# Kernel optimization log

Measured on AMD Instinct MI355X. Metric: run time of the kernel, lower is better.

The kernel has to match this reference:

```python
import jax, jax.numpy as jnp
import numpy as np

B, C, H, W = 4, 64, 64, 64
NUM_HEADS = 4
INTER = 64
OUT_PLANE = 64
TOP_K = 5
BN_EPS = 1e-5


def setup_inputs() -> dict:
    key = jax.random.key(0)
    ks = jax.random.split(key, 24)
    d = {}
    d['x'] = jax.random.normal(ks[0], (B, C, H, W), dtype=jnp.float32)
    oc = INTER * NUM_HEADS
    s_in = 1.0 / np.sqrt(C)
    s_oc = 1.0 / np.sqrt(oc)
    s_op = 1.0 / np.sqrt(OUT_PLANE)
    d['wk'] = jax.random.normal(ks[1], (oc, C), dtype=jnp.float32) * s_in
    d['bk'] = jax.random.normal(ks[2], (oc,), dtype=jnp.float32) * s_in
    d['wq'] = jax.random.normal(ks[3], (oc, C), dtype=jnp.float32) * s_in
    d['bq'] = jax.random.normal(ks[4], (oc,), dtype=jnp.float32) * s_in
    d['wv'] = jax.random.normal(ks[5], (oc, C), dtype=jnp.float32) * s_in
    d['bv'] = jax.random.normal(ks[6], (oc,), dtype=jnp.float32) * s_in
    d['wp'] = jax.random.normal(ks[7], (OUT_PLANE, oc), dtype=jnp.float32) * s_oc
    d['bp'] = jax.random.normal(ks[8], (OUT_PLANE,), dtype=jnp.float32) * s_oc
    d['w1'] = jax.random.normal(ks[9], (OUT_PLANE, OUT_PLANE), dtype=jnp.float32) * s_op
    d['b1'] = jax.random.normal(ks[10], (OUT_PLANE,), dtype=jnp.float32) * s_op
    d['w2'] = jax.random.normal(ks[11], (OUT_PLANE, OUT_PLANE), dtype=jnp.float32) * s_op
    d['b2'] = jax.random.normal(ks[12], (OUT_PLANE,), dtype=jnp.float32) * s_op
    d['g1'] = 1.0 + 0.1 * jax.random.normal(ks[13], (OUT_PLANE,), dtype=jnp.float32)
    d['beta1'] = 0.1 * jax.random.normal(ks[14], (OUT_PLANE,), dtype=jnp.float32)
    d['m1'] = 0.1 * jax.random.normal(ks[15], (OUT_PLANE,), dtype=jnp.float32)
    d['v1'] = 1.0 + 0.1 * jax.random.uniform(ks[16], (OUT_PLANE,), dtype=jnp.float32)
    d['g2'] = 1.0 + 0.1 * jax.random.normal(ks[17], (OUT_PLANE,), dtype=jnp.float32)
    d['beta2'] = 0.1 * jax.random.normal(ks[18], (OUT_PLANE,), dtype=jnp.float32)
    d['m2'] = 0.1 * jax.random.normal(ks[19], (OUT_PLANE,), dtype=jnp.float32)
    d['v2'] = 1.0 + 0.1 * jax.random.uniform(ks[20], (OUT_PLANE,), dtype=jnp.float32)
    return d


def _conv1x1(x, w, b):
    return jnp.einsum('bchw,oc->bohw', x, w) + b[None, :, None, None]


def _l2norm(x, axis):
    n = jnp.sqrt(jnp.sum(x * x, axis=axis, keepdims=True))
    return x / jnp.maximum(n, 1e-12)


def _bn(x, g, be, m, v):
    scale = g / jnp.sqrt(v + BN_EPS)
    return (x - m[None, :, None, None]) * scale[None, :, None, None] + be[None, :, None, None]


def _laplacian(topk_idx, feats):
    # topk_idx: (b, N, K) int32; feats: (b, heads, N, F)
    b, heads, N, Fd = feats.shape
    K = topk_idx.shape[-1]
    src = jnp.repeat(jnp.arange(N), K)  # (N*K,)

    def one(idx, f):  # idx (N,K), f (heads,N,F)
        dst = idx.reshape(-1)  # (N*K,)
        # A = topk edges + self-loops; row degrees (dim=1 sum)
        deg = jnp.zeros((N,), feats.dtype).at[src].add(1.0) + 1.0
        norm = jnp.maximum(deg ** -0.5, 1e-9)
        w = norm[src] * norm[dst]  # (N*K,)
        gathered = f[:, dst, :] * w[None, :, None]  # (heads, N*K, F)
        agg = jax.vmap(lambda g_: jnp.zeros((N, Fd), feats.dtype).at[src].add(g_))(gathered)
        # self-loop contribution (value 1, norm[i]^2)
        return agg + (norm * norm)[None, :, None] * f

    return jax.vmap(one)(topk_idx, feats)


def reference(x, wk, bk, wq, bq, wv, bv, wp, bp, w1, b1, w2, b2,
              g1, beta1, m1, v1, g2, beta2, m2, v2):
    b, c, h, w = x.shape
    N = h * w
    # q/k/v: (b, heads, N, inter)
    k = _conv1x1(x, wk, bk).reshape(b, NUM_HEADS, INTER, N).transpose(0, 1, 3, 2)
    q = _conv1x1(x, wq, bq).reshape(b, NUM_HEADS, INTER, N).transpose(0, 1, 3, 2)
    v = _conv1x1(x, wv, bv).reshape(b, NUM_HEADS, INTER, N).transpose(0, 1, 3, 2)
    k = _l2norm(k, -1)
    q = _l2norm(q, -1)
    # hypergraph: cosine similarity over channels, top-k neighbors per node
    x_flat = x.reshape(b, c, N)
    xn = _l2norm(x_flat, 1)
    sim = jnp.einsum('bcn,bcm->bnm', xn, xn)  # (b, N, N)
    _, idx = jax.lax.top_k(sim, TOP_K)  # (b, N, K)
    k = _laplacian(idx, k)
    v = _laplacian(idx, v)
    # hydra attention: kv summed over nodes, broadcast back over q
    kv = jnp.einsum('bhnf,bhnf->bhf', k, v)[:, :, None, :]  # (b, heads, 1, inter)
    hy = q * kv  # (b, heads, N, inter)
    hy = hy.transpose(0, 1, 3, 2).reshape(b, NUM_HEADS * INTER, h, w)
    out = _conv1x1(hy, wp, bp)
    out = jax.nn.relu(_bn(_conv1x1(out, w1, b1), g1, beta1, m1, v1))
    out = jax.nn.relu(_bn(_conv1x1(out, w2, b2), g2, beta2, m2, v2))
    return out
```

## Files before the change

### kernel.cpp

```cpp
#include <hip/hip_runtime.h>
#include <math.h>

#define NB 4
#define NC 64
#define NN 4096
#define NH 4

typedef __attribute__((ext_vector_type(8))) short bf16x8;
typedef __attribute__((ext_vector_type(4))) float f32x4;

__device__ __forceinline__ unsigned int bf16rne(float v) {
    unsigned int u = __float_as_uint(v);
    return (u + 0x7fffu + ((u >> 16) & 1u)) >> 16;
}

__device__ __forceinline__ void ins5k(unsigned int (&tk)[5], unsigned int key) {
    unsigned int n0 = max(tk[0], key);
    unsigned int n1 = min(tk[0], max(tk[1], key));
    unsigned int n2 = min(tk[1], max(tk[2], key));
    unsigned int n3 = min(tk[2], max(tk[3], key));
    unsigned int n4 = min(tk[3], max(tk[4], key));
    tk[0]=n0; tk[1]=n1; tk[2]=n2; tk[3]=n3; tk[4]=n4;
}

__global__ __launch_bounds__(256) void k_xsplit(const float* __restrict__ x,
                                                unsigned short* __restrict__ hl) {
    int t = blockIdx.x*256 + threadIdx.x;
    int b = t >> 12, n = t & (NN-1);
    const float* xb = x + (size_t)b*NC*NN + n;
    float vals[64];
    float ss = 0.f;
    #pragma unroll
    for (int c = 0; c < NC; ++c) { vals[c] = xb[(size_t)c*NN]; ss += vals[c]*vals[c]; }
    float rn = 1.f / fmaxf(sqrtf(ss), 1e-12f);
    unsigned short* ho = hl + (size_t)t*128;
    #pragma unroll
    for (int g = 0; g < 8; ++g) {
        unsigned int hw[4], lw[4];
        #pragma unroll
        for (int p = 0; p < 4; ++p) {
            float v0 = vals[g*8 + p*2]     * rn;
            float v1 = vals[g*8 + p*2 + 1] * rn;
            unsigned int h0 = bf16rne(v0), h1 = bf16rne(v1);
            float r0 = v0 - __uint_as_float(h0 << 16);
            float r1 = v1 - __uint_as_float(h1 << 16);
            unsigned int l0 = bf16rne(r0), l1 = bf16rne(r1);
            hw[p] = h0 | (h1 << 16);
            lw[p] = l0 | (l1 << 16);
        }
        *(uint4*)(ho + g*8)      = make_uint4(hw[0], hw[1], hw[2], hw[3]);
        *(uint4*)(ho + 64 + g*8) = make_uint4(lw[0], lw[1], lw[2], lw[3]);
    }
}

__global__ __launch_bounds__(256) void k_qkv(
    const float* __restrict__ x,
    const float* __restrict__ wk, const float* __restrict__ bk,
    const float* __restrict__ wq, const float* __restrict__ bq,
    const float* __restrict__ wv, const float* __restrict__ bv,
    float* __restrict__ qo, float* __restrict__ ko, float* __restrict__ vo)
{
    int blk = blockIdx.x;
    int nt  = blk & 63;
    int rem = blk >> 6;
    int ot  = rem % 12;
    int b   = rem / 12;
    int mat = ot >> 2, h = ot & 3;
    const float* w    = (mat==0) ? wk : ((mat==1) ? wq : wv);
    const float* bias = (mat==0) ? bk : ((mat==1) ? bq : bv);
    float* outp       = (mat==0) ? ko : ((mat==1) ? qo : vo);

    __shared__ __align__(16) float As[64*68];
    __shared__ __align__(16) float Bs[64*68];
    __shared__ float redq[16][64];
    __shared__ float rnl[64];
    int t = threadIdx.x;
    int n0 = nt*64;
    {
        int f = t >> 2, q4 = t & 3;
        #pragma unroll
        for (int s = 0; s < 4; ++s) {
            int c0 = q4*16 + s*4;
            float4 w4 = *(const float4*)(w + (size_t)(h*64+f)*64 + c0);
            As[(c0+0)*68+f] = w4.x; As[(c0+1)*68+f] = w4.y;
            As[(c0+2)*68+f] = w4.z; As[(c0+3)*68+f] = w4.w;
        }
    }
    {
        int u = t & 15, cb = t >> 4;
        #pragma unroll
        for (int s = 0; s < 4; ++s) {
            int c = cb + 16*s;
            float4 x4 = *(const float4*)(x + ((size_t)b*NC + c)*NN + n0 + u*4);
            *(float4*)&Bs[c*68 + u*4] = x4;
        }
    }
    __syncthreads();
    int tr = t >> 4, tc = t & 15;
    float acc[4][4];
    #pragma unroll
    for (int i=0;i<4;++i) {
        float bb = bias[h*64 + tr*4 + i];
        #pragma unroll
        for (int j=0;j<4;++j) acc[i][j] = bb;
    }
    #pragma unroll 8
    for (int c = 0; c < 64; ++c) {
        float4 a4 = *(const float4*)&As[c*68 + tr*4];
        float4 b4 = *(const float4*)&Bs[c*68 + tc*4];
        float av[4]  = {a4.x,a4.y,a4.z,a4.w};
        float bvv[4] = {b4.x,b4.y,b4.z,b4.w};
        #pragma unroll
        for (int i=0;i<4;++i)
            #pragma unroll
            for (int j=0;j<4;++j)
                acc[i][j] += av[i]*bvv[j];
    }
    if (mat != 2) {
        #pragma unroll
        for (int j=0;j<4;++j) {
            float s2 = acc[0][j]*acc[0][j] + acc[1][j]*acc[1][j]
                     + acc[2][j]*acc[2][j] + acc[3][j]*acc[3][j];
            redq[tr][tc*4+j] = s2;
        }
        __syncthreads();
        if (t < 64) {
            float s2 = 0.f;
            #pragma unroll
            for (int q = 0; q < 16; ++q) s2 += redq[q][t];
            rnl[t] = 1.f / fmaxf(sqrtf(s2), 1e-12f);
        }
        __syncthreads();
        #pragma unroll
        for (int j=0;j<4;++j) {
            float rr = rnl[tc*4+j];
            #pragma unroll
            for (int i=0;i<4;++i) acc[i][j] *= rr;
        }
    }
    float* ob = outp + (((size_t)(b*NH + h))*NN + n0)*64;
    #pragma unroll
    for (int j=0;j<4;++j) {
        float4 o4 = make_float4(acc[0][j], acc[1][j], acc[2][j], acc[3][j]);
        *(float4*)(ob + (size_t)(tc*4+j)*64 + tr*4) = o4;
    }
}

__device__ __forceinline__ void ctile(const bf16x8& ah0, const bf16x8& ah1,
                                      const bf16x8& al0, const bf16x8& al1,
                                      const bf16x8& bh0, const bf16x8& bh1,
                                      const bf16x8& bl0, const bf16x8& bl1,
                                      unsigned int (&tk)[4][5], unsigned int inv)
{
    f32x4 accP = {2.0f, 2.0f, 2.0f, 2.0f};
    f32x4 accQ = {0.f, 0.f, 0.f, 0.f};
    f32x4 accR = {0.f, 0.f, 0.f, 0.f};
    accP = __builtin_amdgcn_mfma_f32_16x16x32_bf16(ah0, bh0, accP, 0,0,0);
    accQ = __builtin_amdgcn_mfma_f32_16x16x32_bf16(al0, bh0, accQ, 0,0,0);
    accR = __builtin_amdgcn_mfma_f32_16x16x32_bf16(ah0, bl0, accR, 0,0,0);
    accP = __builtin_amdgcn_mfma_f32_16x16x32_bf16(ah1, bh1, accP, 0,0,0);
    accQ = __builtin_amdgcn_mfma_f32_16x16x32_bf16(al1, bh1, accQ, 0,0,0);
    accR = __builtin_amdgcn_mfma_f32_16x16x32_bf16(ah1, bl1, accR, 0,0,0);
    #pragma unroll
    for (int r = 0; r < 4; ++r) {
        float v = (accP[r] + accQ[r]) + accR[r];
        unsigned int key = (__float_as_uint(v) & 0xFFFFF000u) | inv;
        ins5k(tk[r], key);
    }
}

__global__ __launch_bounds__(256, 2)
void k_topk(const unsigned short* __restrict__ hl, unsigned int* __restrict__ pk)
{
    int blk = blockIdx.x;
    int cs = blk & 7;
    int rg = (blk >> 3) & 31;
    int b  = blk >> 8;
    int t = threadIdx.x, lane = t & 63, wave = t >> 6;
    int ln = lane & 15, kh = lane >> 4;
    const unsigned short* hb = hl + (size_t)b*NN*128;

    const unsigned short* ap0 = hb + (size_t)(rg*128 + wave*32 + ln)*128 + kh*8;
    const unsigned short* ap1 = ap0 + 16*128;
    bf16x8 a0h0 = *(const bf16x8*)(ap0);
    bf16x8 a0h1 = *(const bf16x8*)(ap0 + 32);
    bf16x8 a0l0 = *(const bf16x8*)(ap0 + 64);
    bf16x8 a0l1 = *(const bf16x8*)(ap0 + 96);
    bf16x8 a1h0 = *(const bf16x8*)(ap1);
    bf16x8 a1h1 = *(const bf16x8*)(ap1 + 32);
    bf16x8 a1l0 = *(const bf16x8*)(ap1 + 64);
    bf16x8 a1l1 = *(const bf16x8*)(ap1 + 96);

    unsigned int tkA[4][5], tkB[4][5];
    #pragma unroll
    for (int r=0;r<4;++r)
        #pragma unroll
        for (int kk=0;kk<5;++kk) { tkA[r][kk] = 0u; tkB[r][kk] = 0u; }

    int colbase = cs*512;
    unsigned int inv0 = 4095u - (unsigned int)(colbase + ln);

    const unsigned short* bp = hb + (size_t)(colbase + ln)*128 + kh*8;
    bf16x8 Ah0 = *(const bf16x8*)(bp);
    bf16x8 Ah1 = *(const bf16x8*)(bp + 32);
    bf16x8 Al0 = *(const bf16x8*)(bp + 64);
    bf16x8 Al1 = *(const bf16x8*)(bp + 96);
    bf16x8 Bh0, Bh1, Bl0, Bl1;

    for (int t5 = 0; t5 < 32; t5 += 2) {
        {
            const unsigned short* p = bp + (size_t)(t5+1)*16*128;
            Bh0 = *(const bf16x8*)(p);
            Bh1 = *(const bf16x8*)(p + 32);
            Bl0 = *(const bf16x8*)(p + 64);
            Bl1 = *(const bf16x8*)(p + 96);
        }
        {
            unsigned int inv = inv0 - (unsigned int)(t5*16);
            ctile(a0h0,a0h1,a0l0,a0l1, Ah0,Ah1,Al0,Al1, tkA, inv);
            ctile(a1h0,a1h1,a1l0,a1l1, Ah0,Ah1,Al0,Al1, tkB, inv);
        }
        {
            int m = (t5+2 < 32) ? (t5+2) : 0;
            const unsigned short* p = bp + (size_t)m*16*128;
            Ah0 = *(const bf16x8*)(p);
            Ah1 = *(const bf16x8*)(p + 32);
            Al0 = *(const bf16x8*)(p + 64);
            Al1 = *(const bf16x8*)(p + 96);
        }
        {
            unsigned int inv = inv0 - (unsigned int)((t5+1)*16);
            ctile(a0h0,a0h1,a0l0,a0l1, Bh0,Bh1,Bl0,Bl1, tkA, inv);
            ctile(a1h0,a1h1,a1l0,a1l1, Bh0,Bh1,Bl0,Bl1, tkB, inv);
        }
    }

    #pragma unroll
    for (int m = 1; m < 16; m <<= 1) {
        #pragma unroll
        for (int r=0;r<4;++r) {
            unsigned int okA[5], okB[5];
            #pragma unroll
            for (int kk=0;kk<5;++kk) {
                okA[kk] = (unsigned int)__shfl_xor((int)tkA[r][kk], m);
                okB[kk] = (unsigned int)__shfl_xor((int)tkB[r][kk], m);
            }
            #pragma unroll
            for (int kk=0;kk<5;++kk) { ins5k(tkA[r], okA[kk]); ins5k(tkB[r], okB[kk]); }
        }
    }
    if (ln == 0) {
        #pragma unroll
        for (int r=0;r<4;++r) {
            int row0 = rg*128 + wave*32 + kh*4 + r;
            size_t base0 = (((size_t)b*NN + row0)*8 + cs)*5;
            size_t base1 = (((size_t)b*NN + row0 + 16)*8 + cs)*5;
            #pragma unroll
            for (int kk=0;kk<5;++kk) { pk[base0+kk] = tkA[r][kk]; pk[base1+kk] = tkB[r][kk]; }
        }
    }
}

__global__ __launch_bounds__(256) void k_kv(const float* __restrict__ ko, const float* __restrict__ vo,
                                            const unsigned int* __restrict__ pk, float* __restrict__ part)
{
    int blk = blockIdx.x;
    int chunk = blk & 15, bh = blk >> 4, b = bh >> 2;
    int t = threadIdx.x;
    __shared__ int idxl[256][5];
    __shared__ float red[4][64];
    {
        int n = chunk*256 + t;
        const uint4* pp = (const uint4*)(pk + ((size_t)b*NN + n)*40);
        unsigned int bk5[5] = {0u,0u,0u,0u,0u};
        #pragma unroll
        for (int e = 0; e < 10; ++e) {
            uint4 v4 = pp[e];
            ins5k(bk5, v4.x); ins5k(bk5, v4.y); ins5k(bk5, v4.z); ins5k(bk5, v4.w);
        }
        #pragma unroll
        for (int kk=0;kk<5;++kk) idxl[t][kk] = 4095 - (int)(bk5[kk] & 0xFFFu);
    }
    __syncthreads();
    int f = t & 63, g = t >> 6;
    const float* kb = ko + (size_t)bh*NN*64;
    const float* vb = vo + (size_t)bh*NN*64;
    float acc = 0.f;
    for (int i2 = 0; i2 < 64; ++i2) {
        int nl = g*64 + i2;
        int n = chunk*256 + nl;
        const int* ip = idxl[nl];
        int j0 = ip[0], j1 = ip[1], j2 = ip[2], j3 = ip[3], j4 = ip[4];
        float lk = kb[(size_t)n*64+f] + kb[(size_t)j0*64+f] + kb[(size_t)j1*64+f]
                 + kb[(size_t)j2*64+f] + kb[(size_t)j3*64+f] + kb[(size_t)j4*64+f];
        float lv = vb[(size_t)n*64+f] + vb[(size_t)j0*64+f] + vb[(size_t)j1*64+f]
                 + vb[(size_t)j2*64+f] + vb[(size_t)j3*64+f] + vb[(size_t)j4*64+f];
        acc += lk*lv;
    }
    red[g][f] = acc;
    __syncthreads();
    if (t < 64) {
        float s2 = red[0][t] + red[1][t] + red[2][t] + red[3][t];
        part[((size_t)bh*64 + t)*16 + chunk] = s2;
    }
}

__global__ __launch_bounds__(256) void k_out(
    const float* __restrict__ qo, const float* __restrict__ wp, const float* __restrict__ part,
    const float* __restrict__ bp,
    const float* __restrict__ w1, const float* __restrict__ b1,
    const float* __restrict__ w2, const float* __restrict__ b2,
    const float* __restrict__ g1, const float* __restrict__ be1,
    const float* __restrict__ m1, const float* __restrict__ v1,
    const float* __restrict__ g2, const float* __restrict__ be2,
    const float* __restrict__ m2, const float* __restrict__ v2,
    float* __restrict__ outp)
{
    int b  = blockIdx.x >> 6;
    int n0 = (blockIdx.x & 63)*64;
    __shared__ __align__(16) float qs[256*68];
    __shared__ __align__(16) float ws2[256*68];
    __shared__ __align__(16) float t0[64*68];
    int t = threadIdx.x;
    {
        int f = t & 63, sub = t >> 6;
        #pragma unroll
        for (int h = 0; h < 4; ++h) {
            const float* qb = qo + (((size_t)(b*4+h))*NN + n0)*64 + f;
            for (int nl = sub; nl < 64; nl += 4)
                qs[(h*64+f)*68 + nl] = qb[(size_t)nl*64];
        }
    }
    {
        const float* pp = part + ((size_t)b*256 + t)*16;
        float s = 0.f;
        #pragma unroll
        for (int c2 = 0; c2 < 16; ++c2) s += pp[c2];
        float kvv = s * (1.f/36.f);
        for (int o = 0; o < 64; ++o)
            ws2[t*68 + o] = wp[(size_t)o*256 + t] * kvv;
    }
    __syncthreads();
    int tr = t >> 4, tc = t & 15;
    float acc[4][4];
    #pragma unroll
    for (int i=0;i<4;++i) {
        float bb = bp[tr*4+i];
        #pragma unroll
        for (int j=0;j<4;++j) acc[i][j] = bb;
    }
    #pragma unroll 8
    for (int hf = 0; hf < 256; ++hf) {
        float4 a4 = *(const float4*)&ws2[hf*68 + tr*4];
        float4 b4 = *(const float4*)&qs[hf*68 + tc*4];
        float av[4]={a4.x,a4.y,a4.z,a4.w}, bvv[4]={b4.x,b4.y,b4.z,b4.w};
        #pragma unroll
        for (int i=0;i<4;++i)
            #pragma unroll
            for (int j=0;j<4;++j)
                acc[i][j] += av[i]*bvv[j];
    }
    #pragma unroll
    for (int i=0;i<4;++i)
        *(float4*)&t0[(tr*4+i)*68 + tc*4] = make_float4(acc[i][0],acc[i][1],acc[i][2],acc[i][3]);
    __syncthreads();
    #pragma unroll
    for (int s = 0; s < 16; ++s) {
        int e = t + 256*s;
        ws2[(e & 63)*68 + (e >> 6)] = w1[e];
    }
    __syncthreads();
    float acc2[4][4];
    #pragma unroll
    for (int i=0;i<4;++i)
        #pragma unroll
        for (int j=0;j<4;++j) acc2[i][j] = 0.f;
    #pragma unroll 8
    for (int c = 0; c < 64; ++c) {
        float4 a4 = *(const float4*)&ws2[c*68 + tr*4];
        float4 b4 = *(const float4*)&t0[c*68 + tc*4];
        float av[4]={a4.x,a4.y,a4.z,a4.w}, bvv[4]={b4.x,b4.y,b4.z,b4.w};
        #pragma unroll
        for (int i=0;i<4;++i)
            #pragma unroll
            for (int j=0;j<4;++j)
                acc2[i][j] += av[i]*bvv[j];
    }
    #pragma unroll
    for (int i=0;i<4;++i) {
        int o = tr*4+i;
        float sc = g1[o] / sqrtf(v1[o] + 1e-5f);
        float bb = b1[o], mm = m1[o], bt = be1[o];
        float4 r;
        r.x = fmaxf((acc2[i][0]+bb-mm)*sc + bt, 0.f);
        r.y = fmaxf((acc2[i][1]+bb-mm)*sc + bt, 0.f);
        r.z = fmaxf((acc2[i][2]+bb-mm)*sc + bt, 0.f);
        r.w = fmaxf((acc2[i][3]+bb-mm)*sc + bt, 0.f);
        *(float4*)&qs[o*68 + tc*4] = r;
    }
    __syncthreads();
    #pragma unroll
    for (int s = 0; s < 16; ++s) {
        int e = t + 256*s;
        ws2[(e & 63)*68 + (e >> 6)] = w2[e];
    }
    __syncthreads();
    float acc3[4][4];
    #pragma unroll
    for (int i=0;i<4;++i)
        #pragma unroll
        for (int j=0;j<4;++j) acc3[i][j] = 0.f;
    #pragma unroll 8
    for (int c = 0; c < 64; ++c) {
        float4 a4 = *(const float4*)&ws2[c*68 + tr*4];
        float4 b4 = *(const float4*)&qs[c*68 + tc*4];
        float av[4]={a4.x,a4.y,a4.z,a4.w}, bvv[4]={b4.x,b4.y,b4.z,b4.w};
        #pragma unroll
        for (int i=0;i<4;++i)
            #pragma unroll
            for (int j=0;j<4;++j)
                acc3[i][j] += av[i]*bvv[j];
    }
    #pragma unroll
    for (int i=0;i<4;++i) {
        int o = tr*4+i;
        float sc = g2[o] / sqrtf(v2[o] + 1e-5f);
        float bb = b2[o], mm = m2[o], bt = be2[o];
        float4 r;
        r.x = fmaxf((acc3[i][0]+bb-mm)*sc + bt, 0.f);
        r.y = fmaxf((acc3[i][1]+bb-mm)*sc + bt, 0.f);
        r.z = fmaxf((acc3[i][2]+bb-mm)*sc + bt, 0.f);
        r.w = fmaxf((acc3[i][3]+bb-mm)*sc + bt, 0.f);
        *(float4*)&t0[o*68 + tc*4] = r;
    }
    __syncthreads();
    float* ob = outp + ((size_t)b*64)*NN + n0;
    #pragma unroll
    for (int s = 0; s < 16; ++s) {
        int e = t + 256*s;
        int o = e >> 6, nl = e & 63;
        ob[(size_t)o*NN + nl] = t0[o*68 + nl];
    }
}

extern "C" void kernel_launch(void* const* d_in, const int* in_sizes, int n_in,
                              void* d_out, int out_size, void* d_ws, size_t ws_size,
                              hipStream_t stream)
{
    (void)in_sizes; (void)n_in; (void)out_size; (void)ws_size;
    const float* x  = (const float*)d_in[0];
    const float* wk = (const float*)d_in[1];
    const float* bk = (const float*)d_in[2];
    const float* wq = (const float*)d_in[3];
    const float* bq = (const float*)d_in[4];
    const float* wv = (const float*)d_in[5];
    const float* bv = (const float*)d_in[6];
    const float* wp = (const float*)d_in[7];
    const float* bp = (const float*)d_in[8];
    const float* w1 = (const float*)d_in[9];
    const float* b1 = (const float*)d_in[10];
    const float* w2 = (const float*)d_in[11];
    const float* b2 = (const float*)d_in[12];
    const float* g1 = (const float*)d_in[13];
    const float* be1= (const float*)d_in[14];
    const float* m1 = (const float*)d_in[15];
    const float* v1 = (const float*)d_in[16];
    const float* g2 = (const float*)d_in[17];
    const float* be2= (const float*)d_in[18];
    const float* m2 = (const float*)d_in[19];
    const float* v2 = (const float*)d_in[20];
    float* out = (float*)d_out;

    float* ws = (float*)d_ws;
    unsigned short* hlb = (unsigned short*)ws;  ws += (size_t)NB*NN*128/2;
    float* qbuf = ws;  ws += (size_t)NB*NH*NN*64;
    float* kbuf = ws;  ws += (size_t)NB*NH*NN*64;
    float* vbuf = ws;  ws += (size_t)NB*NH*NN*64;
    float* part = ws;  ws += (size_t)16*64*16;
    unsigned int* pk = (unsigned int*)ws;  ws += (size_t)NB*NN*40;

    k_xsplit<<<64, 256, 0, stream>>>(x, hlb);
    k_qkv<<<3072, 256, 0, stream>>>(x, wk,bk, wq,bq, wv,bv, qbuf,kbuf,vbuf);
    k_topk<<<1024, 256, 0, stream>>>(hlb, pk);
    k_kv<<<256, 256, 0, stream>>>(kbuf, vbuf, pk, part);
    k_out<<<256, 256, 0, stream>>>(qbuf, wp, part, bp, w1,b1, w2,b2,
                                   g1,be1,m1,v1, g2,be2,m2,v2, out);
}
```

Baseline: 155.2 us.

## Compute QKV projection with split-bf16 MFMA instead of fp32 FMA

```diff
diff --git a/kernel.cpp b/kernel.cpp
--- a/kernel.cpp
+++ b/kernel.cpp
@@ -23,8 +23,51 @@
     tk[0]=n0; tk[1]=n1; tk[2]=n2; tk[3]=n3; tk[4]=n4;
 }
 
+__device__ __forceinline__ void split8(const float* v, uint4& hw4, uint4& lw4) {
+    unsigned int hw[4], lw[4];
+    #pragma unroll
+    for (int p = 0; p < 4; ++p) {
+        float v0 = v[p*2], v1 = v[p*2+1];
+        unsigned int h0 = bf16rne(v0), h1 = bf16rne(v1);
+        float r0 = v0 - __uint_as_float(h0 << 16);
+        float r1 = v1 - __uint_as_float(h1 << 16);
+        unsigned int l0 = bf16rne(r0), l1 = bf16rne(r1);
+        hw[p] = h0 | (h1 << 16);
+        lw[p] = l0 | (l1 << 16);
+    }
+    hw4 = make_uint4(hw[0], hw[1], hw[2], hw[3]);
+    lw4 = make_uint4(lw[0], lw[1], lw[2], lw[3]);
+}
+
 __global__ __launch_bounds__(256) void k_xsplit(const float* __restrict__ x,
-                                                unsigned short* __restrict__ hl) {
+                                                const float* __restrict__ wk,
+                                                const float* __restrict__ wq,
+                                                const float* __restrict__ wv,
+                                                unsigned short* __restrict__ hl,
+                                                unsigned short* __restrict__ xr,
+                                                unsigned short* __restrict__ wsb) {
+    if (blockIdx.x == 64) {
+        int t = threadIdx.x;
+        #pragma unroll
+        for (int rr = 0; rr < 3; ++rr) {
+            int r = t + rr*256;
+            int mat = r >> 8, oc = r & 255;
+            const float* wsrc = (mat==0) ? wk : ((mat==1) ? wq : wv);
+            float wrow[64];
+            #pragma unroll
+            for (int g = 0; g < 16; ++g)
+                *(float4*)&wrow[g*4] = *(const float4*)(wsrc + (size_t)oc*64 + g*4);
+            unsigned short* wo = wsb + (size_t)r*128;
+            #pragma unroll
+            for (int g = 0; g < 8; ++g) {
+                uint4 hw4, lw4;
+                split8(&wrow[g*8], hw4, lw4);
+                *(uint4*)(wo + g*8)      = hw4;
+                *(uint4*)(wo + 64 + g*8) = lw4;
+            }
+        }
+        return;
+    }
     int t = blockIdx.x*256 + threadIdx.x;
     int b = t >> 12, n = t & (NN-1);
     const float* xb = x + (size_t)b*NC*NN + n;
@@ -34,115 +77,92 @@
     for (int c = 0; c < NC; ++c) { vals[c] = xb[(size_t)c*NN]; ss += vals[c]*vals[c]; }
     float rn = 1.f / fmaxf(sqrtf(ss), 1e-12f);
     unsigned short* ho = hl + (size_t)t*128;
+    unsigned short* ro = xr + (size_t)t*128;
     #pragma unroll
     for (int g = 0; g < 8; ++g) {
-        unsigned int hw[4], lw[4];
-        #pragma unroll
-        for (int p = 0; p < 4; ++p) {
-            float v0 = vals[g*8 + p*2]     * rn;
-            float v1 = vals[g*8 + p*2 + 1] * rn;
-            unsigned int h0 = bf16rne(v0), h1 = bf16rne(v1);
-            float r0 = v0 - __uint_as_float(h0 << 16);
-            float r1 = v1 - __uint_as_float(h1 << 16);
-            unsigned int l0 = bf16rne(r0), l1 = bf16rne(r1);
-            hw[p] = h0 | (h1 << 16);
-            lw[p] = l0 | (l1 << 16);
-        }
-        *(uint4*)(ho + g*8)      = make_uint4(hw[0], hw[1], hw[2], hw[3]);
-        *(uint4*)(ho + 64 + g*8) = make_uint4(lw[0], lw[1], lw[2], lw[3]);
-    }
-}
-
-__global__ __launch_bounds__(256) void k_qkv(
-    const float* __restrict__ x,
-    const float* __restrict__ wk, const float* __restrict__ bk,
-    const float* __restrict__ wq, const float* __restrict__ bq,
-    const float* __restrict__ wv, const float* __restrict__ bv,
+        float nv[8];
+        #pragma unroll
+        for (int p = 0; p < 8; ++p) nv[p] = vals[g*8+p] * rn;
+        uint4 hw4, lw4;
+        split8(nv, hw4, lw4);
+        *(uint4*)(ho + g*8)      = hw4;
+        *(uint4*)(ho + 64 + g*8) = lw4;
+        split8(&vals[g*8], hw4, lw4);
+        *(uint4*)(ro + g*8)      = hw4;
+        *(uint4*)(ro + 64 + g*8) = lw4;
+    }
+}
+
+__global__ __launch_bounds__(256, 2) void k_qkv(
+    const unsigned short* __restrict__ xr, const unsigned short* __restrict__ wsb,
+    const float* __restrict__ bk, const float* __restrict__ bq, const float* __restrict__ bv,
     float* __restrict__ qo, float* __restrict__ ko, float* __restrict__ vo)
 {
     int blk = blockIdx.x;
     int nt  = blk & 63;
     int rem = blk >> 6;
-    int ot  = rem % 12;
-    int b   = rem / 12;
-    int mat = ot >> 2, h = ot & 3;
-    const float* w    = (mat==0) ? wk : ((mat==1) ? wq : wv);
+    int mat = rem % 3, b = rem / 3;
     const float* bias = (mat==0) ? bk : ((mat==1) ? bq : bv);
     float* outp       = (mat==0) ? ko : ((mat==1) ? qo : vo);
-
-    __shared__ __align__(16) float As[64*68];
-    __shared__ __align__(16) float Bs[64*68];
-    __shared__ float redq[16][64];
-    __shared__ float rnl[64];
-    int t = threadIdx.x;
-    int n0 = nt*64;
-    {
-        int f = t >> 2, q4 = t & 3;
+    int t = threadIdx.x, lane = t & 63, h = t >> 6;
+    int ln = lane & 15, kh = lane >> 4;
+
+    bf16x8 ah0[4], ah1[4], al0[4], al1[4];
+    const unsigned short* wb2 = wsb + ((size_t)(mat*256 + h*64 + ln))*128 + kh*8;
+    #pragma unroll
+    for (int s = 0; s < 4; ++s) {
+        const unsigned short* p = wb2 + (size_t)s*16*128;
+        ah0[s] = *(const bf16x8*)(p);
+        ah1[s] = *(const bf16x8*)(p + 32);
+        al0[s] = *(const bf16x8*)(p + 64);
+        al1[s] = *(const bf16x8*)(p + 96);
+    }
+    float4 bj[4];
+    #pragma unroll
+    for (int s = 0; s < 4; ++s) bj[s] = *(const float4*)(bias + h*64 + s*16 + kh*4);
+
+    int n0base = nt*64;
+    const unsigned short* xb2 = xr + ((size_t)b*NN + n0base + ln)*128 + kh*8;
+    #pragma unroll
+    for (int j = 0; j < 4; ++j) {
+        const unsigned short* p = xb2 + (size_t)j*16*128;
+        bf16x8 bh0 = *(const bf16x8*)(p);
+        bf16x8 bh1 = *(const bf16x8*)(p + 32);
+        bf16x8 bl0 = *(const bf16x8*)(p + 64);
+        bf16x8 bl1 = *(const bf16x8*)(p + 96);
+        f32x4 av[4];
         #pragma unroll
         for (int s = 0; s < 4; ++s) {
-            int c0 = q4*16 + s*4;
-            float4 w4 = *(const float4*)(w + (size_t)(h*64+f)*64 + c0);
-            As[(c0+0)*68+f] = w4.x; As[(c0+1)*68+f] = w4.y;
-            As[(c0+2)*68+f] = w4.z; As[(c0+3)*68+f] = w4.w;
-        }
-    }
-    {
-        int u = t & 15, cb = t >> 4;
-        #pragma unroll
-        for (int s = 0; s < 4; ++s) {
-            int c = cb + 16*s;
-            float4 x4 = *(const float4*)(x + ((size_t)b*NC + c)*NN + n0 + u*4);
-            *(float4*)&Bs[c*68 + u*4] = x4;
-        }
-    }
-    __syncthreads();
-    int tr = t >> 4, tc = t & 15;
-    float acc[4][4];
-    #pragma unroll
-    for (int i=0;i<4;++i) {
-        float bb = bias[h*64 + tr*4 + i];
-        #pragma unroll
-        for (int j=0;j<4;++j) acc[i][j] = bb;
-    }
-    #pragma unroll 8
-    for (int c = 0; c < 64; ++c) {
-        float4 a4 = *(const float4*)&As[c*68 + tr*4];
-        float4 b4 = *(const float4*)&Bs[c*68 + tc*4];
-        float av[4]  = {a4.x,a4.y,a4.z,a4.w};
-        float bvv[4] = {b4.x,b4.y,b4.z,b4.w};
-        #pragma unroll
-        for (int i=0;i<4;++i)
-            #pragma unroll
-            for (int j=0;j<4;++j)
-                acc[i][j] += av[i]*bvv[j];
-    }
-    if (mat != 2) {
-        #pragma unroll
-        for (int j=0;j<4;++j) {
-            float s2 = acc[0][j]*acc[0][j] + acc[1][j]*acc[1][j]
-                     + acc[2][j]*acc[2][j] + acc[3][j]*acc[3][j];
-            redq[tr][tc*4+j] = s2;
-        }
-        __syncthreads();
-        if (t < 64) {
-            float s2 = 0.f;
-            #pragma unroll
-            for (int q = 0; q < 16; ++q) s2 += redq[q][t];
-            rnl[t] = 1.f / fmaxf(sqrtf(s2), 1e-12f);
-        }
-        __syncthreads();
-        #pragma unroll
-        for (int j=0;j<4;++j) {
-            float rr = rnl[tc*4+j];
-            #pragma unroll
-            for (int i=0;i<4;++i) acc[i][j] *= rr;
-        }
-    }
-    float* ob = outp + (((size_t)(b*NH + h))*NN + n0)*64;
-    #pragma unroll
-    for (int j=0;j<4;++j) {
-        float4 o4 = make_float4(acc[0][j], acc[1][j], acc[2][j], acc[3][j]);
-        *(float4*)(ob + (size_t)(tc*4+j)*64 + tr*4) = o4;
+            f32x4 acc = {bj[s].x, bj[s].y, bj[s].z, bj[s].w};
+            acc = __builtin_amdgcn_mfma_f32_16x16x32_bf16(ah0[s], bh0, acc, 0,0,0);
+            acc = __builtin_amdgcn_mfma_f32_16x16x32_bf16(ah1[s], bh1, acc, 0,0,0);
+            acc = __builtin_amdgcn_mfma_f32_16x16x32_bf16(al0[s], bh0, acc, 0,0,0);
+            acc = __builtin_amdgcn_mfma_f32_16x16x32_bf16(al1[s], bh1, acc, 0,0,0);
+            acc = __builtin_amdgcn_mfma_f32_16x16x32_bf16(ah0[s], bl0, acc, 0,0,0);
+            acc = __builtin_amdgcn_mfma_f32_16x16x32_bf16(ah1[s], bl1, acc, 0,0,0);
+            av[s] = acc;
+        }
+        int n = n0base + j*16 + ln;
+        float* ob = outp + (((size_t)(b*NH + h))*NN + n)*64 + kh*4;
+        if (mat != 2) {
+            float ss = 0.f;
+            #pragma unroll
+            for (int s = 0; s < 4; ++s)
+                ss += av[s][0]*av[s][0] + av[s][1]*av[s][1]
+                    + av[s][2]*av[s][2] + av[s][3]*av[s][3];
+            ss += __shfl_xor(ss, 16);
+            ss += __shfl_xor(ss, 32);
+            float rn = 1.f / fmaxf(sqrtf(ss), 1e-12f);
+            #pragma unroll
+            for (int s = 0; s < 4; ++s)
+                *(float4*)(ob + s*16) = make_float4(av[s][0]*rn, av[s][1]*rn,
+                                                    av[s][2]*rn, av[s][3]*rn);
+        } else {
+            #pragma unroll
+            for (int s = 0; s < 4; ++s)
+                *(float4*)(ob + s*16) = make_float4(av[s][0], av[s][1],
+                                                    av[s][2], av[s][3]);
+        }
     }
 }
 
@@ -473,14 +493,16 @@
 
     float* ws = (float*)d_ws;
     unsigned short* hlb = (unsigned short*)ws;  ws += (size_t)NB*NN*128/2;
+    unsigned short* xrb = (unsigned short*)ws;  ws += (size_t)NB*NN*128/2;
+    unsigned short* wsb = (unsigned short*)ws;  ws += (size_t)768*128/2;
     float* qbuf = ws;  ws += (size_t)NB*NH*NN*64;
     float* kbuf = ws;  ws += (size_t)NB*NH*NN*64;
     float* vbuf = ws;  ws += (size_t)NB*NH*NN*64;
     float* part = ws;  ws += (size_t)16*64*16;
     unsigned int* pk = (unsigned int*)ws;  ws += (size_t)NB*NN*40;
 
-    k_xsplit<<<64, 256, 0, stream>>>(x, hlb);
-    k_qkv<<<3072, 256, 0, stream>>>(x, wk,bk, wq,bq, wv,bv, qbuf,kbuf,vbuf);
+    k_xsplit<<<65, 256, 0, stream>>>(x, wk, wq, wv, hlb, xrb, wsb);
+    k_qkv<<<768, 256, 0, stream>>>(xrb, wsb, bk, bq, bv, qbuf, kbuf, vbuf);
     k_topk<<<1024, 256, 0, stream>>>(hlb, pk);
     k_kv<<<256, 256, 0, stream>>>(kbuf, vbuf, pk, part);
     k_out<<<256, 256, 0, stream>>>(qbuf, wp, part, bp, w1,b1, w2,b2,
```

Measured after the change: 159.2 us. +2.6%, slower.
